# Optimization experiments

Measured on AMD Instinct MI355X. Metric: run time of the kernel, lower is better.

The kernel has to match this reference:

```python
import jax, jax.numpy as jnp
import numpy as np

N, E, F_IN, HID, L, G = 50000, 800000, 128, 64, 3, 512
BN_EPS = 1e-5


def setup_inputs() -> dict:
    key = jax.random.key(0)
    ks = jax.random.split(key, 8)
    x = jax.random.normal(ks[0], (N, F_IN), dtype=jnp.float32)
    edge_index = jax.random.randint(ks[1], (2, E), 0, N, dtype=jnp.int32)
    batch = jnp.sort(jax.random.randint(ks[2], (N,), 0, G, dtype=jnp.int32))
    # params (Glorot-ish init for weights; BN init per module: gamma=1, beta=1e-4)
    W_feat = jax.random.normal(ks[3], (F_IN, HID), dtype=jnp.float32) / np.sqrt(F_IN)
    b_feat = jnp.zeros((HID,), jnp.float32)
    Ws = jax.random.normal(ks[4], (L, HID, HID), dtype=jnp.float32) / np.sqrt(HID)
    bs = jnp.zeros((L, HID), jnp.float32)
    bn_feat_g = jnp.ones((F_IN,), jnp.float32)
    bn_feat_b = jnp.full((F_IN,), 1e-4, jnp.float32)
    bn_g = jnp.ones((L, HID), jnp.float32)
    bn_b = jnp.full((L, HID), 1e-4, jnp.float32)
    return {"x": x, "edge_index": edge_index, "batch": batch,
            "bn_feat_g": bn_feat_g, "bn_feat_b": bn_feat_b,
            "W_feat": W_feat, "b_feat": b_feat,
            "bn_g": bn_g, "bn_b": bn_b, "Ws": Ws, "bs": bs}


def batch_norm(x, gamma, beta):
    # training-mode BatchNorm1d: biased variance over the node dimension
    mu = jnp.mean(x, axis=0)
    var = jnp.mean(jnp.square(x - mu), axis=0)
    return (x - mu) * jax.lax.rsqrt(var + BN_EPS) * gamma + beta


def gcn_conv(h, W, b, src, dst):
    # h: [N, d_in] -> linear then normalized gather-scatter with self-loops
    h = h @ W  # [N, d_out]
    n = h.shape[0]
    loop = jnp.arange(n, dtype=src.dtype)
    row = jnp.concatenate([src, loop])  # source (j)
    col = jnp.concatenate([dst, loop])  # target (i)
    w = jnp.ones(row.shape[0], h.dtype)
    deg = jax.ops.segment_sum(w, row, num_segments=n)  # PyG: deg over row
    dis = jnp.where(deg > 0, jax.lax.rsqrt(jnp.maximum(deg, 1.0)), 0.0)
    norm = dis[row] * w * dis[col]  # [E+N]
    out = jax.ops.segment_sum(norm[:, None] * h[row], col, num_segments=n)
    return out + b


def reference(x, edge_index, batch, bn_feat_g, bn_feat_b, W_feat, b_feat,
              bn_g, bn_b, Ws, bs):
    src, dst = edge_index[0], edge_index[1]
    h = batch_norm(x, bn_feat_g, bn_feat_b)
    h = jax.nn.relu(h @ W_feat + b_feat)  # conv_feat has gfn=True -> plain linear
    for i in range(L):
        h = batch_norm(h, bn_g[i], bn_b[i])
        h = jax.nn.relu(gcn_conv(h, Ws[i], bs[i], src, dst))
    graph_emb = jax.ops.segment_sum(h, batch, num_segments=G)  # global_add_pool
    return graph_emb
```

## Files before the change

kernel.cpp:

```cpp
#include <hip/hip_runtime.h>
#include <math.h>

#define HID 64
#define BN_EPS 1e-5f
#define NREP 64

typedef unsigned int uint;
typedef unsigned short ushort;


__device__ inline uint bf16pk(float a, float b) {
    uint ua = __builtin_bit_cast(uint, a);
    ua += 0x7fff + ((ua >> 16) & 1);
    uint ub = __builtin_bit_cast(uint, b);
    ub += 0x7fff + ((ub >> 16) & 1);
    return (ua >> 16) | (ub & 0xffff0000u);
}
__device__ inline float bfl(uint v) { return __builtin_bit_cast(float, v << 16); }
__device__ inline float bfh(uint v) { return __builtin_bit_cast(float, v & 0xffff0000u); }


__global__ __launch_bounds__(256) void k_scatter_stats(
        const int* __restrict__ ei, int E, int NB, int SCB, int C,
        int* __restrict__ cursor_d, int* __restrict__ cursor_s,
        uint* __restrict__ bedge, int* __restrict__ bsrc,
        const float* __restrict__ X, int n, float* __restrict__ stats) {
    __shared__ __align__(16) char smemraw[8192];
    int t = threadIdx.x;
    if ((int)blockIdx.x < SCB) {
        int* hd = (int*)smemraw;
        int* hs = hd + 256;
        int* curd = hs + 256;
        int* curs = curd + 256;
        int chunk = (E + SCB - 1) / SCB;
        int e0 = blockIdx.x * chunk;
        int e1 = min(e0 + chunk, E);
        if (t < NB) { hd[t] = 0; hs[t] = 0; }
        __syncthreads();
        for (int e = e0 + t; e < e1; e += 256) {
            int src = ei[e], dst = ei[E + e];
            atomicAdd(&hd[dst >> 8], 1);
            atomicAdd(&hs[src >> 8], 1);
        }
        __syncthreads();
        if (t < NB) {
            curd[t] = hd[t] ? atomicAdd(&cursor_d[t], hd[t]) : 0;
            curs[t] = hs[t] ? atomicAdd(&cursor_s[t], hs[t]) : 0;
        }
        __syncthreads();
        for (int e = e0 + t; e < e1; e += 256) {
            int src = ei[e], dst = ei[E + e];
            int bd = dst >> 8, bsr = src >> 8;
            int pd = atomicAdd(&curd[bd], 1);
            if (pd < C) bedge[(size_t)bd * C + pd] = ((uint)(dst & 255) << 16) | (uint)src;
            int ps = atomicAdd(&curs[bsr], 1);
            if (ps < C) bsrc[(size_t)bsr * C + ps] = src;
        }
    } else {
        int b = blockIdx.x - SCB;
        int SB = gridDim.x - SCB;
        float4* shs = (float4*)smemraw;
        float4* shq = shs + 256;
        int c4 = t & 31, rsub = t >> 5;
        float4 s = make_float4(0.f, 0.f, 0.f, 0.f);
        float4 q = make_float4(0.f, 0.f, 0.f, 0.f);
        for (int r = b * 8 + rsub; r < n; r += SB * 8) {
            float4 v = ((const float4*)X)[(size_t)r * 32 + c4];
            s.x += v.x; s.y += v.y; s.z += v.z; s.w += v.w;
            q.x = fmaf(v.x, v.x, q.x); q.y = fmaf(v.y, v.y, q.y);
            q.z = fmaf(v.z, v.z, q.z); q.w = fmaf(v.w, v.w, q.w);
        }
        shs[t] = s; shq[t] = q;
        __syncthreads();
        if (rsub == 0) {
            #pragma unroll
            for (int k = 1; k < 8; k++) {
                float4 a = shs[t + k * 32], bq = shq[t + k * 32];
                s.x += a.x; s.y += a.y; s.z += a.z; s.w += a.w;
                q.x += bq.x; q.y += bq.y; q.z += bq.z; q.w += bq.w;
            }
            float* sb = stats + ((int)blockIdx.x & (NREP - 1)) * 256;
            atomicAdd(&sb[4 * t + 0], s.x); atomicAdd(&sb[4 * t + 1], s.y);
            atomicAdd(&sb[4 * t + 2], s.z); atomicAdd(&sb[4 * t + 3], s.w);
            atomicAdd(&sb[128 + 4 * t + 0], q.x); atomicAdd(&sb[128 + 4 * t + 1], q.y);
            atomicAdd(&sb[128 + 4 * t + 2], q.z); atomicAdd(&sb[128 + 4 * t + 3], q.w);
        }
    }
}


template <int K, bool RELU, bool DIS, bool STATS, bool HASB>
__device__ __forceinline__ void gemm_body(const float* __restrict__ X, const float* __restrict__ W,
                                          const float* __restrict__ stats,
                                          const float* __restrict__ gamma, const float* __restrict__ beta,
                                          const float* __restrict__ bias0, const float* __restrict__ dis,
                                          float n_inv, void* __restrict__ out, int n,
                                          float* __restrict__ sout, int bx) {
    constexpr int KC = 64;
    constexpr int XS = 68;
    constexpr int NSUB = 256 / K;
    __shared__ float Xs[KC * XS];
    __shared__ float Wsm[KC * HID];
    __shared__ float As[128], Cs[128];

    int t = threadIdx.x;
    int tx = t & 15, ty = t >> 4;
    int row0 = bx * 64;

    {
        int f = t & (K - 1);
        int sub = t / K;
        float ssum = 0.f, qsum = 0.f;
        const float* sp = stats + f;
        #pragma unroll 4
        for (int r = sub; r < NREP; r += NSUB) {
            ssum += sp[(size_t)r * 2 * K];
            qsum += sp[(size_t)r * 2 * K + K];
        }
        Xs[t] = ssum;
        Xs[256 + t] = qsum;
    }
    __syncthreads();
    if (t < K) {
        float ss = 0.f, qq = 0.f;
        #pragma unroll
        for (int s = 0; s < NSUB; ++s) { ss += Xs[s * K + t]; qq += Xs[256 + s * K + t]; }
        float mu = ss * n_inv;
        float var = qq * n_inv - mu * mu;
        float a = gamma[t] * rsqrtf(var + BN_EPS);
        As[t] = a;
        Cs[t] = beta[t] - mu * a;
    }
    __syncthreads();

    float acc[4][4];
    #pragma unroll
    for (int i = 0; i < 4; i++)
        #pragma unroll
        for (int j = 0; j < 4; j++) acc[i][j] = 0.f;
    float4 bp = make_float4(0.f, 0.f, 0.f, 0.f);

    for (int kc = 0; kc < K; kc += KC) {
        #pragma unroll
        for (int it = 0; it < 4; ++it) {
            int id = t + 256 * it;
            int r = id >> 4, c4 = id & 15;
            float4 v = make_float4(0.f, 0.f, 0.f, 0.f);
            if (row0 + r < n) v = *(const float4*)(X + (size_t)(row0 + r) * K + kc + 4 * c4);
            int kk = 4 * c4;
            Xs[(kk + 0) * XS + r] = v.x;
            Xs[(kk + 1) * XS + r] = v.y;
            Xs[(kk + 2) * XS + r] = v.z;
            Xs[(kk + 3) * XS + r] = v.w;
        }
        {
            const float4* wsrc = (const float4*)(W + (size_t)kc * HID);
            #pragma unroll
            for (int it = 0; it < 4; ++it) {
                int id = t + 256 * it;
                int kl = id >> 4;
                float4 raw = wsrc[id];
                float a = As[kc + kl], c = Cs[kc + kl];
                float4 sc;
                sc.x = a * raw.x; sc.y = a * raw.y; sc.z = a * raw.z; sc.w = a * raw.w;
                ((float4*)Wsm)[id] = sc;
                bp.x = fmaf(c, raw.x, bp.x);
                bp.y = fmaf(c, raw.y, bp.y);
                bp.z = fmaf(c, raw.z, bp.z);
                bp.w = fmaf(c, raw.w, bp.w);
            }
        }
        __syncthreads();
        #pragma unroll 8
        for (int k = 0; k < KC; ++k) {
            float4 xv = *(const float4*)&Xs[k * XS + 4 * ty];
            float4 wv = *(const float4*)&Wsm[k * HID + 4 * tx];
            acc[0][0] = fmaf(xv.x, wv.x, acc[0][0]);
            acc[0][1] = fmaf(xv.x, wv.y, acc[0][1]);
            acc[0][2] = fmaf(xv.x, wv.z, acc[0][2]);
            acc[0][3] = fmaf(xv.x, wv.w, acc[0][3]);
            acc[1][0] = fmaf(xv.y, wv.x, acc[1][0]);
            acc[1][1] = fmaf(xv.y, wv.y, acc[1][1]);
            acc[1][2] = fmaf(xv.y, wv.z, acc[1][2]);
            acc[1][3] = fmaf(xv.y, wv.w, acc[1][3]);
            acc[2][0] = fmaf(xv.z, wv.x, acc[2][0]);
            acc[2][1] = fmaf(xv.z, wv.y, acc[2][1]);
            acc[2][2] = fmaf(xv.z, wv.z, acc[2][2]);
            acc[2][3] = fmaf(xv.z, wv.w, acc[2][3]);
            acc[3][0] = fmaf(xv.w, wv.x, acc[3][0]);
            acc[3][1] = fmaf(xv.w, wv.y, acc[3][1]);
            acc[3][2] = fmaf(xv.w, wv.z, acc[3][2]);
            acc[3][3] = fmaf(xv.w, wv.w, acc[3][3]);
        }
        __syncthreads();
    }

    {
        float* redb = Xs + 2048;
        *(float4*)&redb[ty * 64 + 4 * tx] = bp;
        __syncthreads();
        if (t < 64) {
            float s = 0.f;
            #pragma unroll
            for (int k = 0; k < 16; ++k) s += redb[k * 64 + t];
            Xs[3072 + t] = s + (HASB ? bias0[t] : 0.f);
        }
        __syncthreads();
    }
    float4 bv = *(const float4*)&Xs[3072 + 4 * tx];

    float4 cs = make_float4(0.f, 0.f, 0.f, 0.f);
    float4 cq = make_float4(0.f, 0.f, 0.f, 0.f);
    #pragma unroll
    for (int i = 0; i < 4; ++i) {
        int row = row0 + 4 * ty + i;
        bool valid = row < n;
        float vx = acc[i][0] + bv.x, vy = acc[i][1] + bv.y;
        float vz = acc[i][2] + bv.z, vw = acc[i][3] + bv.w;
        if constexpr (DIS) {
            if (valid) {
                float d = dis[row];
                uint2 pk;
                pk.x = bf16pk(vx * d, vy * d);
                pk.y = bf16pk(vz * d, vw * d);
                *(uint2*)((ushort*)out + (size_t)row * HID + 4 * tx) = pk;
            }
        } else {
            float4 v;
            v.x = RELU ? fmaxf(vx, 0.f) : vx;
            v.y = RELU ? fmaxf(vy, 0.f) : vy;
            v.z = RELU ? fmaxf(vz, 0.f) : vz;
            v.w = RELU ? fmaxf(vw, 0.f) : vw;
            if (valid) {
                *(float4*)((float*)out + (size_t)row * HID + 4 * tx) = v;
                if constexpr (STATS) {
                    cs.x += v.x; cs.y += v.y; cs.z += v.z; cs.w += v.w;
                    cq.x = fmaf(v.x, v.x, cq.x); cq.y = fmaf(v.y, v.y, cq.y);
                    cq.z = fmaf(v.z, v.z, cq.z); cq.w = fmaf(v.w, v.w, cq.w);
                }
            }
        }
    }
    if constexpr (STATS) {
        __syncthreads();
        float* reds = Xs;
        float* redq = Xs + 1024;
        *(float4*)&reds[ty * 64 + 4 * tx] = cs;
        *(float4*)&redq[ty * 64 + 4 * tx] = cq;
        __syncthreads();
        if (t < 64) {
            float s = 0.f, q = 0.f;
            #pragma unroll
            for (int k = 0; k < 16; ++k) { s += reds[k * 64 + t]; q += redq[k * 64 + t]; }
            float* sb = sout + (bx & (NREP - 1)) * 128;
            atomicAdd(&sb[t], s);
            atomicAdd(&sb[64 + t], q);
        }
    }
}

template <int K, bool RELU, bool DIS, bool STATS, bool HASB>
__global__ __launch_bounds__(256) void k_gemm(const float* __restrict__ X, const float* __restrict__ W,
                                              const float* __restrict__ stats,
                                              const float* __restrict__ gamma, const float* __restrict__ beta,
                                              const float* __restrict__ bias0, const float* __restrict__ dis,
                                              float n_inv, void* __restrict__ out, int n,
                                              float* __restrict__ sout) {
    gemm_body<K, RELU, DIS, STATS, HASB>(X, W, stats, gamma, beta, bias0, dis, n_inv, out, n, sout,
                                         (int)blockIdx.x);
}


__global__ __launch_bounds__(256) void k_dis_gemm(
        const int* __restrict__ bsrc, const int* __restrict__ cursor_s, int C, int N, int NB,
        float* __restrict__ dis,
        const float* __restrict__ X, const float* __restrict__ W,
        const float* __restrict__ stats,
        const float* __restrict__ gamma, const float* __restrict__ beta,
        const float* __restrict__ bias0,
        float n_inv, void* __restrict__ out, int n, float* __restrict__ sout) {
    int t = threadIdx.x, b = blockIdx.x;
    if (b < NB) {
        __shared__ int h[256];
        int base = b * C;
        int end = base + min(cursor_s[b], C);
        h[t] = 0; __syncthreads();
        for (int p = base + t; p < end; p += 256) atomicAdd(&h[bsrc[p] & 255], 1);
        __syncthreads();
        int node = (b << 8) + t;
        if (node < N) dis[node] = rsqrtf((float)(h[t] + 1));
    } else {
        gemm_body<128, true, false, true, true>(X, W, stats, gamma, beta, bias0, nullptr,
                                                n_inv, out, n, sout, b - NB);
    }
}


__global__ __launch_bounds__(256) void k_fill_gemm(
        const uint* __restrict__ bedge, const int* __restrict__ cursor_d, int C, int N, int NB,
        int* __restrict__ rowptr, int* __restrict__ deg, int* __restrict__ eidx,
        const float* __restrict__ X, const float* __restrict__ W,
        const float* __restrict__ stats,
        const float* __restrict__ gamma, const float* __restrict__ beta,
        const float* __restrict__ dis,
        float n_inv, void* __restrict__ out, int n) {
    int t = threadIdx.x, b = blockIdx.x;
    if (b < NB) {
        __shared__ int h[256], off[256], cur[256];
        int base = b * C;
        int cnt = min(cursor_d[b], C);
        int end = base + cnt;
        h[t] = 0; __syncthreads();
        for (int p = base + t; p < end; p += 256)
            atomicAdd(&h[(int)(bedge[p] >> 16) & 255], 1);
        __syncthreads();
        off[t] = h[t]; __syncthreads();
        for (int s = 1; s < 256; s <<= 1) { int u = (t >= s) ? off[t - s] : 0; __syncthreads(); off[t] += u; __syncthreads(); }
        int excl = off[t] - h[t];
        int node = (b << 8) + t;
        if (node < N) { rowptr[node] = base + excl; deg[node] = h[t]; }
        cur[t] = excl; __syncthreads();
        for (int p = base + t; p < end; p += 256) {
            uint be = bedge[p];
            int bin = (int)(be >> 16) & 255;
            int pos = atomicAdd(&cur[bin], 1);
            eidx[base + pos] = (int)(be & 0xffffu);
        }
    } else {
        gemm_body<64, false, true, false, false>(X, W, stats, gamma, beta, nullptr, dis,
                                                 n_inv, out, n, nullptr, b - NB);
    }
}


template <bool POOL>
__global__ __launch_bounds__(256) void k_agg(const ushort* __restrict__ s, const int* __restrict__ rowptr,
                                             const int* __restrict__ deg,
                                             const int* __restrict__ eidx, const float* __restrict__ dis,
                                             const float* __restrict__ bias, float* __restrict__ out, int n,
                                             float* __restrict__ sout, const int* __restrict__ batch,
                                             float* __restrict__ pool_out) {
    __shared__ float shs[8 * 64];
    __shared__ float shq[8 * 64];
    __shared__ int ib[8];
    int t = threadIdx.x;
    int nl = t >> 5;
    int li = t & 31;
    int slot = li >> 3;
    int c = li & 7;
    int i = blockIdx.x * 8 + nl;
    const uint4* sp4 = (const uint4*)s;
    float a[8];
    #pragma unroll
    for (int k = 0; k < 8; ++k) a[k] = 0.f;
    bool valid = i < n;
    if (valid) {
        int q0 = rowptr[i];
        int qe = q0 + deg[i];
        int q = q0 + slot;
        while (q < qe) {
            int qm = qe - 1;
            int q1 = q + 4, q2 = q + 8, q3 = q + 12;
            bool p1 = q1 < qe, p2 = q2 < qe, p3 = q3 < qe;
            int j0 = eidx[q];
            int j1 = eidx[min(q1, qm)];
            int j2 = eidx[min(q2, qm)];
            int j3 = eidx[min(q3, qm)];
            if (!p1) j1 = i;
            if (!p2) j2 = i;
            if (!p3) j3 = i;
            uint4 v0 = sp4[(size_t)j0 * 8 + c];
            uint4 v1 = sp4[(size_t)j1 * 8 + c];
            uint4 v2 = sp4[(size_t)j2 * 8 + c];
            uint4 v3 = sp4[(size_t)j3 * 8 + c];
            float m1 = p1 ? 1.f : 0.f;
            float m2 = p2 ? 1.f : 0.f;
            float m3 = p3 ? 1.f : 0.f;
            q += 16;
            a[0] += bfl(v0.x); a[1] += bfh(v0.x);
            a[2] += bfl(v0.y); a[3] += bfh(v0.y);
            a[4] += bfl(v0.z); a[5] += bfh(v0.z);
            a[6] += bfl(v0.w); a[7] += bfh(v0.w);
            a[0] = fmaf(m1, bfl(v1.x), a[0]); a[1] = fmaf(m1, bfh(v1.x), a[1]);
            a[2] = fmaf(m1, bfl(v1.y), a[2]); a[3] = fmaf(m1, bfh(v1.y), a[3]);
            a[4] = fmaf(m1, bfl(v1.z), a[4]); a[5] = fmaf(m1, bfh(v1.z), a[5]);
            a[6] = fmaf(m1, bfl(v1.w), a[6]); a[7] = fmaf(m1, bfh(v1.w), a[7]);
            a[0] = fmaf(m2, bfl(v2.x), a[0]); a[1] = fmaf(m2, bfh(v2.x), a[1]);
            a[2] = fmaf(m2, bfl(v2.y), a[2]); a[3] = fmaf(m2, bfh(v2.y), a[3]);
            a[4] = fmaf(m2, bfl(v2.z), a[4]); a[5] = fmaf(m2, bfh(v2.z), a[5]);
            a[6] = fmaf(m2, bfl(v2.w), a[6]); a[7] = fmaf(m2, bfh(v2.w), a[7]);
            a[0] = fmaf(m3, bfl(v3.x), a[0]); a[1] = fmaf(m3, bfh(v3.x), a[1]);
            a[2] = fmaf(m3, bfl(v3.y), a[2]); a[3] = fmaf(m3, bfh(v3.y), a[3]);
            a[4] = fmaf(m3, bfl(v3.z), a[4]); a[5] = fmaf(m3, bfh(v3.z), a[5]);
            a[6] = fmaf(m3, bfl(v3.w), a[6]); a[7] = fmaf(m3, bfh(v3.w), a[7]);
        }
    }
    #pragma unroll
    for (int k = 0; k < 8; ++k) a[k] += __shfl_xor(a[k], 8);
    #pragma unroll
    for (int k = 0; k < 8; ++k) a[k] += __shfl_xor(a[k], 16);

    if (li < 8) {
        float r[8];
        if (valid) {
            uint4 v = sp4[(size_t)i * 8 + c];
            a[0] += bfl(v.x); a[1] += bfh(v.x);
            a[2] += bfl(v.y); a[3] += bfh(v.y);
            a[4] += bfl(v.z); a[5] += bfh(v.z);
            a[6] += bfl(v.w); a[7] += bfh(v.w);
            float d = dis[i];
            float4 b0 = *(const float4*)(bias + 8 * c);
            float4 b1 = *(const float4*)(bias + 8 * c + 4);
            r[0] = fmaxf(fmaf(d, a[0], b0.x), 0.f);
            r[1] = fmaxf(fmaf(d, a[1], b0.y), 0.f);
            r[2] = fmaxf(fmaf(d, a[2], b0.z), 0.f);
            r[3] = fmaxf(fmaf(d, a[3], b0.w), 0.f);
            r[4] = fmaxf(fmaf(d, a[4], b1.x), 0.f);
            r[5] = fmaxf(fmaf(d, a[5], b1.y), 0.f);
            r[6] = fmaxf(fmaf(d, a[6], b1.z), 0.f);
            r[7] = fmaxf(fmaf(d, a[7], b1.w), 0.f);
            if constexpr (!POOL) {
                *(float4*)(out + (size_t)i * HID + 8 * c)     = make_float4(r[0], r[1], r[2], r[3]);
                *(float4*)(out + (size_t)i * HID + 8 * c + 4) = make_float4(r[4], r[5], r[6], r[7]);
            }
        } else {
            #pragma unroll
            for (int k = 0; k < 8; ++k) r[k] = 0.f;
        }
        #pragma unroll
        for (int k = 0; k < 8; ++k) shs[nl * 64 + 8 * c + k] = r[k];
        if constexpr (!POOL) {
            #pragma unroll
            for (int k = 0; k < 8; ++k) shq[nl * 64 + 8 * c + k] = r[k] * r[k];
        }
    }
    if constexpr (POOL) {
        if (li == 0) ib[nl] = valid ? batch[i] : -1;
    }
    __syncthreads();
    if (t < 64) {
        if constexpr (!POOL) {
            float ss = 0.f, qq = 0.f;
            #pragma unroll
            for (int k = 0; k < 8; ++k) { ss += shs[k * 64 + t]; qq += shq[k * 64 + t]; }
            float* sb = sout + ((int)blockIdx.x & (NREP - 1)) * 128;
            atomicAdd(&sb[t], ss);
            atomicAdd(&sb[64 + t], qq);
        } else {
            int g = ib[0];
            float run = shs[t];
            #pragma unroll
            for (int k = 1; k < 8; ++k) {
                int gk = ib[k];
                float v = shs[k * 64 + t];
                if (gk == g) {
                    run += v;
                } else {
                    if (g >= 0) atomicAdd(&pool_out[(size_t)g * HID + t], run);
                    g = gk; run = v;
                }
            }
            if (g >= 0) atomicAdd(&pool_out[(size_t)g * HID + t], run);
        }
    }
}


extern "C" void kernel_launch(void* const* d_in, const int* in_sizes, int n_in,
                              void* d_out, int out_size, void* d_ws, size_t ws_size,
                              hipStream_t stream) {
    const float* x     = (const float*)d_in[0];
    const int*   ei    = (const int*)d_in[1];
    const int*   batch = (const int*)d_in[2];
    const float* bnfg  = (const float*)d_in[3];
    const float* bnfb  = (const float*)d_in[4];
    const float* Wfeat = (const float*)d_in[5];
    const float* bfeat = (const float*)d_in[6];
    const float* bng   = (const float*)d_in[7];
    const float* bnb   = (const float*)d_in[8];
    const float* Ws    = (const float*)d_in[9];
    const float* bs    = (const float*)d_in[10];
    float* out = (float*)d_out;

    const int N   = in_sizes[2];
    const int E   = in_sizes[1] / 2;
    const int L   = in_sizes[9] / (HID * HID);
    const int NB  = (N + 255) >> 8;
    const int C   = (E + NB - 1) / NB + 1024;
    const int SB  = 512;
    const int SCB = 256;
    const int gG  = (N + 63) / 64;
    const int gA  = (N + 7) / 8;
    const float n_inv = 1.f / (float)N;

    char* w = (char*)d_ws;
    auto alloc = [&](size_t bytes) { char* p = w; w += (bytes + 255) & ~(size_t)255; return p; };
    int*   cursor_d = (int*)alloc(256 * 4);
    int*   cursor_s = (int*)alloc(256 * 4);
    float* statsX   = (float*)alloc((size_t)NREP * 256 * 4);
    float* statsL   = (float*)alloc((size_t)3 * NREP * 128 * 4);
    size_t zero_bytes = (size_t)(w - (char*)d_ws);
    int*   rowptr = (int*)alloc((size_t)N * 4);
    int*   deg    = (int*)alloc((size_t)N * 4);
    int*   eidx   = (int*)alloc((size_t)NB * C * 4);
    float* dis    = (float*)alloc((size_t)N * 4);
    float* bufA   = (float*)alloc((size_t)N * HID * 4);
    ushort* bufB  = (ushort*)alloc((size_t)N * HID * 2);
    uint*  bedge  = (uint*)alloc((size_t)NB * C * 4);
    int*   bsrc   = (int*)alloc((size_t)NB * C * 4);

    hipMemsetAsync(d_ws, 0, zero_bytes, stream);
    hipMemsetAsync(d_out, 0, (size_t)out_size * sizeof(float), stream);

    k_scatter_stats<<<SCB + SB, 256, 0, stream>>>(ei, E, NB, SCB, C, cursor_d, cursor_s,
                                                  bedge, bsrc, x, N, statsX);
    k_dis_gemm<<<NB + gG, 256, 0, stream>>>(bsrc, cursor_s, C, N, NB, dis,
                                            x, Wfeat, statsX, bnfg, bnfb, bfeat,
                                            n_inv, (void*)bufA, N, statsL);
    k_fill_gemm<<<NB + gG, 256, 0, stream>>>(bedge, cursor_d, C, N, NB, rowptr, deg, eidx,
                                             bufA, Ws, statsL, bng, bnb, dis,
                                             n_inv, (void*)bufB, N);
    k_agg<false><<<gA, 256, 0, stream>>>(bufB, rowptr, deg, eidx, dis, bs,
                                         bufA, N, statsL + (size_t)1 * NREP * 128,
                                         nullptr, nullptr);

    for (int l = 1; l < L; ++l) {
        k_gemm<64, false, true, false, false><<<gG, 256, 0, stream>>>(
            bufA, Ws + (size_t)l * HID * HID, statsL + (size_t)l * NREP * 128,
            bng + (size_t)l * HID, bnb + (size_t)l * HID,
            nullptr, dis, n_inv, (void*)bufB, N, nullptr);
        if (l < L - 1) {
            k_agg<false><<<gA, 256, 0, stream>>>(bufB, rowptr, deg, eidx, dis, bs + (size_t)l * HID,
                                                 bufA, N, statsL + (size_t)(l + 1) * NREP * 128,
                                                 nullptr, nullptr);
        } else {
            k_agg<true><<<gA, 256, 0, stream>>>(bufB, rowptr, deg, eidx, dis, bs + (size_t)l * HID,
                                                nullptr, N, nullptr, batch, out);
        }
    }
}
```

Before: 240.3 us.

## Split bf16 feature buffer into two half-width planes and aggregate per half

The GEMM epilogue now writes its bf16 output as two separate 32-feature planes, and the aggregation kernel launches twice as many blocks, each gathering only one half. Each neighbor row fetch drops from 128 to 64 bytes, so each half plane is smaller and more of it can stay in cache during the random gathers. In exchange the edge index list is read twice and there are twice as many stats and pool atomics. Per-lane edge parallelism rises from 4 to 8 slots.

Measured after the change: 258.6 us. 1.08x slower.

```diff
diff --git a/kernel.cpp b/kernel.cpp
--- a/kernel.cpp
+++ b/kernel.cpp
@@ -94,8 +94,8 @@
                                           const float* __restrict__ stats,
                                           const float* __restrict__ gamma, const float* __restrict__ beta,
                                           const float* __restrict__ bias0, const float* __restrict__ dis,
-                                          float n_inv, void* __restrict__ out, int n,
-                                          float* __restrict__ sout, int bx) {
+                                          float n_inv, void* __restrict__ out, void* __restrict__ out2,
+                                          int n, float* __restrict__ sout, int bx) {
     constexpr int KC = 64;
     constexpr int XS = 68;
     constexpr int NSUB = 256 / K;
@@ -223,7 +223,10 @@
                 uint2 pk;
                 pk.x = bf16pk(vx * d, vy * d);
                 pk.y = bf16pk(vz * d, vw * d);
-                *(uint2*)((ushort*)out + (size_t)row * HID + 4 * tx) = pk;
+                ushort* dstp = (tx < 8)
+                    ? ((ushort*)out  + (size_t)row * 32 + 4 * tx)
+                    : ((ushort*)out2 + (size_t)row * 32 + 4 * (tx - 8));
+                *(uint2*)dstp = pk;
             }
         } else {
             float4 v;
@@ -264,10 +267,10 @@
                                               const float* __restrict__ stats,
                                               const float* __restrict__ gamma, const float* __restrict__ beta,
                                               const float* __restrict__ bias0, const float* __restrict__ dis,
-                                              float n_inv, void* __restrict__ out, int n,
-                                              float* __restrict__ sout) {
-    gemm_body<K, RELU, DIS, STATS, HASB>(X, W, stats, gamma, beta, bias0, dis, n_inv, out, n, sout,
-                                         (int)blockIdx.x);
+                                              float n_inv, void* __restrict__ out, void* __restrict__ out2,
+                                              int n, float* __restrict__ sout) {
+    gemm_body<K, RELU, DIS, STATS, HASB>(X, W, stats, gamma, beta, bias0, dis, n_inv, out, out2,
+                                         n, sout, (int)blockIdx.x);
 }
 
 
@@ -291,7 +294,7 @@
         if (node < N) dis[node] = rsqrtf((float)(h[t] + 1));
     } else {
         gemm_body<128, true, false, true, true>(X, W, stats, gamma, beta, bias0, nullptr,
-                                                n_inv, out, n, sout, b - NB);
+                                                n_inv, out, nullptr, n, sout, b - NB);
     }
 }
 
@@ -303,7 +306,7 @@
         const float* __restrict__ stats,
         const float* __restrict__ gamma, const float* __restrict__ beta,
         const float* __restrict__ dis,
-        float n_inv, void* __restrict__ out, int n) {
+        float n_inv, void* __restrict__ out, void* __restrict__ out2, int n) {
     int t = threadIdx.x, b = blockIdx.x;
     if (b < NB) {
         __shared__ int h[256], off[256], cur[256];
@@ -328,28 +331,31 @@
         }
     } else {
         gemm_body<64, false, true, false, false>(X, W, stats, gamma, beta, nullptr, dis,
-                                                 n_inv, out, n, nullptr, b - NB);
+                                                 n_inv, out, out2, n, nullptr, b - NB);
     }
 }
 
 
 template <bool POOL>
-__global__ __launch_bounds__(256) void k_agg(const ushort* __restrict__ s, const int* __restrict__ rowptr,
-                                             const int* __restrict__ deg,
+__global__ __launch_bounds__(256) void k_agg(const ushort* __restrict__ s0, const ushort* __restrict__ s1,
+                                             const int* __restrict__ rowptr, const int* __restrict__ deg,
                                              const int* __restrict__ eidx, const float* __restrict__ dis,
                                              const float* __restrict__ bias, float* __restrict__ out, int n,
                                              float* __restrict__ sout, const int* __restrict__ batch,
                                              float* __restrict__ pool_out) {
-    __shared__ float shs[8 * 64];
-    __shared__ float shq[8 * 64];
+    __shared__ float shs[8 * 32];
+    __shared__ float shq[8 * 32];
     __shared__ int ib[8];
+    int bid = (int)blockIdx.x;
+    int half = bid & 1;
+    int vb = bid >> 1;
+    const uint4* sp4 = (const uint4*)(half ? s1 : s0);
     int t = threadIdx.x;
     int nl = t >> 5;
     int li = t & 31;
-    int slot = li >> 3;
-    int c = li & 7;
-    int i = blockIdx.x * 8 + nl;
-    const uint4* sp4 = (const uint4*)s;
+    int slot = li >> 2;
+    int c = li & 3;
+    int i = vb * 8 + nl;
     float a[8];
     #pragma unroll
     for (int k = 0; k < 8; ++k) a[k] = 0.f;
@@ -360,7 +366,7 @@
         int q = q0 + slot;
         while (q < qe) {
             int qm = qe - 1;
-            int q1 = q + 4, q2 = q + 8, q3 = q + 12;
+            int q1 = q + 8, q2 = q + 16, q3 = q + 24;
             bool p1 = q1 < qe, p2 = q2 < qe, p3 = q3 < qe;
             int j0 = eidx[q];
             int j1 = eidx[min(q1, qm)];
@@ -369,14 +375,14 @@
             if (!p1) j1 = i;
             if (!p2) j2 = i;
             if (!p3) j3 = i;
-            uint4 v0 = sp4[(size_t)j0 * 8 + c];
-            uint4 v1 = sp4[(size_t)j1 * 8 + c];
-            uint4 v2 = sp4[(size_t)j2 * 8 + c];
-            uint4 v3 = sp4[(size_t)j3 * 8 + c];
+            uint4 v0 = sp4[(size_t)j0 * 4 + c];
+            uint4 v1 = sp4[(size_t)j1 * 4 + c];
+            uint4 v2 = sp4[(size_t)j2 * 4 + c];
+            uint4 v3 = sp4[(size_t)j3 * 4 + c];
             float m1 = p1 ? 1.f : 0.f;
             float m2 = p2 ? 1.f : 0.f;
             float m3 = p3 ? 1.f : 0.f;
-            q += 16;
+            q += 32;
             a[0] += bfl(v0.x); a[1] += bfh(v0.x);
             a[2] += bfl(v0.y); a[3] += bfh(v0.y);
             a[4] += bfl(v0.z); a[5] += bfh(v0.z);
@@ -396,21 +402,24 @@
         }
     }
     #pragma unroll
+    for (int k = 0; k < 8; ++k) a[k] += __shfl_xor(a[k], 4);
+    #pragma unroll
     for (int k = 0; k < 8; ++k) a[k] += __shfl_xor(a[k], 8);
     #pragma unroll
     for (int k = 0; k < 8; ++k) a[k] += __shfl_xor(a[k], 16);
 
-    if (li < 8) {
+    if (li < 4) {
         float r[8];
         if (valid) {
-            uint4 v = sp4[(size_t)i * 8 + c];
+            uint4 v = sp4[(size_t)i * 4 + li];
             a[0] += bfl(v.x); a[1] += bfh(v.x);
             a[2] += bfl(v.y); a[3] += bfh(v.y);
             a[4] += bfl(v.z); a[5] += bfh(v.z);
             a[6] += bfl(v.w); a[7] += bfh(v.w);
             float d = dis[i];
-            float4 b0 = *(const float4*)(bias + 8 * c);
-            float4 b1 = *(const float4*)(bias + 8 * c + 4);
+            const float* bb = bias + half * 32 + 8 * li;
+            float4 b0 = *(const float4*)bb;
+            float4 b1 = *(const float4*)(bb + 4);
             r[0] = fmaxf(fmaf(d, a[0], b0.x), 0.f);
             r[1] = fmaxf(fmaf(d, a[1], b0.y), 0.f);
             r[2] = fmaxf(fmaf(d, a[2], b0.z), 0.f);
@@ -420,47 +429,49 @@
             r[6] = fmaxf(fmaf(d, a[6], b1.z), 0.f);
             r[7] = fmaxf(fmaf(d, a[7], b1.w), 0.f);
             if constexpr (!POOL) {
-                *(float4*)(out + (size_t)i * HID + 8 * c)     = make_float4(r[0], r[1], r[2], r[3]);
-                *(float4*)(out + (size_t)i * HID + 8 * c + 4) = make_float4(r[4], r[5], r[6], r[7]);
+                float* op = out + (size_t)i * HID + half * 32 + 8 * li;
+                *(float4*)op       = make_float4(r[0], r[1], r[2], r[3]);
+                *(float4*)(op + 4) = make_float4(r[4], r[5], r[6], r[7]);
             }
         } else {
             #pragma unroll
             for (int k = 0; k < 8; ++k) r[k] = 0.f;
         }
         #pragma unroll
-        for (int k = 0; k < 8; ++k) shs[nl * 64 + 8 * c + k] = r[k];
+        for (int k = 0; k < 8; ++k) shs[nl * 32 + 8 * li + k] = r[k];
         if constexpr (!POOL) {
             #pragma unroll
-            for (int k = 0; k < 8; ++k) shq[nl * 64 + 8 * c + k] = r[k] * r[k];
+            for (int k = 0; k < 8; ++k) shq[nl * 32 + 8 * li + k] = r[k] * r[k];
         }
     }
     if constexpr (POOL) {
         if (li == 0) ib[nl] = valid ? batch[i] : -1;
     }
     __syncthreads();
-    if (t < 64) {
+    if (t < 32) {
+        int f = half * 32 + t;
         if constexpr (!POOL) {
             float ss = 0.f, qq = 0.f;
             #pragma unroll
-            for (int k = 0; k < 8; ++k) { ss += shs[k * 64 + t]; qq += shq[k * 64 + t]; }
-            float* sb = sout + ((int)blockIdx.x & (NREP - 1)) * 128;
-            atomicAdd(&sb[t], ss);
-            atomicAdd(&sb[64 + t], qq);
+            for (int k = 0; k < 8; ++k) { ss += shs[k * 32 + t]; qq += shq[k * 32 + t]; }
+            float* sb = sout + (vb & (NREP - 1)) * 128;
+            atomicAdd(&sb[f], ss);
+            atomicAdd(&sb[64 + f], qq);
         } else {
             int g = ib[0];
             float run = shs[t];
             #pragma unroll
             for (int k = 1; k < 8; ++k) {
                 int gk = ib[k];
-                float v = shs[k * 64 + t];
+                float v = shs[k * 32 + t];
                 if (gk == g) {
                     run += v;
                 } else {
-                    if (g >= 0) atomicAdd(&pool_out[(size_t)g * HID + t], run);
+                    if (g >= 0) atomicAdd(&pool_out[(size_t)g * HID + f], run);
                     g = gk; run = v;
                 }
             }
-            if (g >= 0) atomicAdd(&pool_out[(size_t)g * HID + t], run);
+            if (g >= 0) atomicAdd(&pool_out[(size_t)g * HID + f], run);
         }
     }
 }
@@ -505,7 +516,8 @@
     int*   eidx   = (int*)alloc((size_t)NB * C * 4);
     float* dis    = (float*)alloc((size_t)N * 4);
     float* bufA   = (float*)alloc((size_t)N * HID * 4);
-    ushort* bufB  = (ushort*)alloc((size_t)N * HID * 2);
+    ushort* bufB0 = (ushort*)alloc((size_t)N * 32 * 2);
+    ushort* bufB1 = (ushort*)alloc((size_t)N * 32 * 2);
     uint*  bedge  = (uint*)alloc((size_t)NB * C * 4);
     int*   bsrc   = (int*)alloc((size_t)NB * C * 4);
 
@@ -519,23 +531,25 @@
                                             n_inv, (void*)bufA, N, statsL);
     k_fill_gemm<<<NB + gG, 256, 0, stream>>>(bedge, cursor_d, C, N, NB, rowptr, deg, eidx,
                                              bufA, Ws, statsL, bng, bnb, dis,
-                                             n_inv, (void*)bufB, N);
-    k_agg<false><<<gA, 256, 0, stream>>>(bufB, rowptr, deg, eidx, dis, bs,
-                                         bufA, N, statsL + (size_t)1 * NREP * 128,
-                                         nullptr, nullptr);
+                                             n_inv, (void*)bufB0, (void*)bufB1, N);
+    k_agg<false><<<2 * gA, 256, 0, stream>>>(bufB0, bufB1, rowptr, deg, eidx, dis, bs,
+                                             bufA, N, statsL + (size_t)1 * NREP * 128,
+                                             nullptr, nullptr);
 
     for (int l = 1; l < L; ++l) {
         k_gemm<64, false, true, false, false><<<gG, 256, 0, stream>>>(
             bufA, Ws + (size_t)l * HID * HID, statsL + (size_t)l * NREP * 128,
             bng + (size_t)l * HID, bnb + (size_t)l * HID,
-            nullptr, dis, n_inv, (void*)bufB, N, nullptr);
+            nullptr, dis, n_inv, (void*)bufB0, (void*)bufB1, N, nullptr);
         if (l < L - 1) {
-            k_agg<false><<<gA, 256, 0, stream>>>(bufB, rowptr, deg, eidx, dis, bs + (size_t)l * HID,
-                                                 bufA, N, statsL + (size_t)(l + 1) * NREP * 128,
-                                                 nullptr, nullptr);
+            k_agg<false><<<2 * gA, 256, 0, stream>>>(bufB0, bufB1, rowptr, deg, eidx, dis,
+                                                     bs + (size_t)l * HID,
+                                                     bufA, N, statsL + (size_t)(l + 1) * NREP * 128,
+                                                     nullptr, nullptr);
         } else {
-            k_agg<true><<<gA, 256, 0, stream>>>(bufB, rowptr, deg, eidx, dis, bs + (size_t)l * HID,
-                                                nullptr, N, nullptr, batch, out);
-        }
-    }
-}
+            k_agg<true><<<2 * gA, 256, 0, stream>>>(bufB0, bufB1, rowptr, deg, eidx, dis,
+                                                    bs + (size_t)l * HID,
+                                                    nullptr, N, nullptr, batch, out);
+        }
+    }
+}
```
